# Optimization experiments

Hardware: AMD Instinct MI355X
Metric: run time of the kernel (lower is better)

The kernel has to match this reference:

```python
import jax, jax.numpy as jnp
import numpy as np

# --- static configuration (Octo-base-ish) ---
B, H, MAXH = 2, 5, 10
NT, NP, NW, NR = 16, 256, 64, 1   # task-lang, obs-primary, obs-wrist, readout tokens
DIN, D, NH, DH = 512, 768, 12, 64
L, DF = 12, 3072
PT = NP + NW + NR                  # tokens per timestep
S = NT + H * PT                    # total sequence length = 1621


def _ln(x, s, b):
    m = x.mean(-1, keepdims=True)
    v = ((x - m) ** 2).mean(-1, keepdims=True)
    return (x - m) * jax.lax.rsqrt(v + 1e-6) * s + b


def _pattern():
    # group ids: 0=task, 1=obs_primary, 2=obs_wrist, 3=readout_action
    gid = np.concatenate([np.zeros(NT, np.int32),
                          np.tile(np.concatenate([np.full(NP, 1), np.full(NW, 2), np.full(NR, 3)]).astype(np.int32), H)])
    ts = np.concatenate([np.full(NT, -1, np.int32), np.repeat(np.arange(H, dtype=np.int32), PT)])
    # attention rules: task->task; obs->{task,obs}; readout->{task,obs,own readout}; nobody attends readouts
    R = np.array([[1, 0, 0, 0],
                  [1, 1, 1, 0],
                  [1, 1, 1, 0],
                  [1, 1, 1, 1]], dtype=bool)
    return jnp.asarray(R[gid[:, None], gid[None, :]] & (ts[None, :] <= ts[:, None]))


def setup_inputs() -> dict:
    key = jax.random.key(0)
    ks = iter(jax.random.split(key, 40))
    n = lambda shape, s=0.02: jax.random.normal(next(ks), shape, jnp.float32) * s
    return dict(
        task_tokens=n((B, NT, DIN), 1.0),
        obs_primary=n((B, H, NP, DIN), 1.0),
        obs_wrist=n((B, H, NW, DIN), 1.0),
        W_task=n((DIN, D)), b_task=jnp.zeros((D,)),
        W_primary=n((DIN, D)), b_primary=jnp.zeros((D,)),
        W_wrist=n((DIN, D)), b_wrist=jnp.zeros((D,)),
        pos_task=n((1, NT, D)), pos_primary=n((1, MAXH, NP, D)),
        pos_wrist=n((1, MAXH, NW, D)), pos_readout=n((1, MAXH, NR, D)),
        ln1_s=jnp.ones((L, D)), ln1_b=jnp.zeros((L, D)),
        Wq=n((L, D, D)), bq=jnp.zeros((L, D)),
        Wk=n((L, D, D)), bk=jnp.zeros((L, D)),
        Wv=n((L, D, D)), bv=jnp.zeros((L, D)),
        Wo=n((L, D, D)), bo=jnp.zeros((L, D)),
        ln2_s=jnp.ones((L, D)), ln2_b=jnp.zeros((L, D)),
        W1=n((L, D, DF)), b1=jnp.zeros((L, DF)),
        W2=n((L, DF, D)), b2=jnp.zeros((L, D)),
        lnf_s=jnp.ones((D,)), lnf_b=jnp.zeros((D,)),
        pad_mask=jnp.ones((B, H), jnp.bool_),
    )


def reference(task_tokens, obs_primary, obs_wrist,
              W_task, b_task, W_primary, b_primary, W_wrist, b_wrist,
              pos_task, pos_primary, pos_wrist, pos_readout,
              ln1_s, ln1_b, Wq, bq, Wk, bk, Wv, bv, Wo, bo,
              ln2_s, ln2_b, W1, b1, W2, b2, lnf_s, lnf_b, pad_mask):
    # --- token group assembly: project + positional embed each group ---
    task_e = task_tokens @ W_task + b_task + pos_task                       # [B,NT,D]
    prim_e = obs_primary @ W_primary + b_primary + pos_primary[:, :H]       # [B,H,NP,D]
    wrist_e = obs_wrist @ W_wrist + b_wrist + pos_wrist[:, :H]              # [B,H,NW,D]
    ro_e = jnp.broadcast_to(pos_readout[:, :H], (B, H, NR, D))              # zeros + pos emb
    step = jnp.concatenate([prim_e, wrist_e, ro_e], axis=2).reshape(B, H * PT, D)
    x = jnp.concatenate([task_e, step], axis=1)                             # [B,S,D]
    # --- key validity mask (pad_mask applies to obs groups; readouts always valid) ---
    km_step = jnp.concatenate([
        jnp.broadcast_to(pad_mask[:, :, None], (B, H, NP + NW)),
        jnp.ones((B, H, NR), bool)], axis=2).reshape(B, H * PT)
    key_mask = jnp.concatenate([jnp.ones((B, NT), bool), km_step], axis=1)  # [B,S]
    mask = _pattern()[None] & key_mask[:, None, :]                          # [B,S,S]
    scale = np.float32(1.0 / np.sqrt(DH))

    params = (ln1_s, ln1_b, Wq, bq, Wk, bk, Wv, bv, Wo, bo, ln2_s, ln2_b, W1, b1, W2, b2)

    def block(h, p):
        s1, t1, wq, bq_, wk, bk_, wv, bv_, wo, bo_, s2, t2, w1, b1_, w2, b2_ = p
        y = _ln(h, s1, t1)
        q = (y @ wq + bq_).reshape(B, S, NH, DH)
        k = (y @ wk + bk_).reshape(B, S, NH, DH)
        v = (y @ wv + bv_).reshape(B, S, NH, DH)
        sc = jnp.einsum('bqhd,bkhd->bhqk', q, k) * scale
        sc = jnp.where(mask[:, None], sc, jnp.float32(-1e9))
        a = jax.nn.softmax(sc, axis=-1)
        o = jnp.einsum('bhqk,bkhd->bqhd', a, v).reshape(B, S, D)
        h = h + o @ wo + bo_
        y2 = _ln(h, s2, t2)
        h = h + jax.nn.gelu(y2 @ w1 + b1_) @ w2 + b2_
        return h, None

    x, _ = jax.lax.scan(block, x, params)
    return _ln(x, lnf_s, lnf_b)  # [B,S,D]: [task | per-t (obs_primary, obs_wrist, readout)]
```

## Files before the change

kernel.cpp:

```cpp
#include <hip/hip_runtime.h>
#include <hip/hip_bf16.h>
#include <math.h>

#define Bb   2
#define Hh   5
#define NTT  16
#define NPP  256
#define NWW  64
#define NRR  1
#define PTT  321
#define SS   1621
#define SSP  1664
#define DINN 512
#define DD   768
#define NHH  12
#define DHH  64
#define LL   12
#define DFF  3072
#define MM   3242
#define MPAD 3328
#define QKVN 2304
#define EROWS 3232

typedef __hip_bfloat16 bf16;
typedef _Float16 f16;
typedef __attribute__((ext_vector_type(4))) float  f32x4;
typedef __attribute__((ext_vector_type(8))) __bf16 bf16x8;
typedef __attribute__((ext_vector_type(8))) _Float16 f16x8;

__device__ __forceinline__ void gid_ts(int i, int& g, int& t) {
  if (i < NTT) { g = 0; t = -1; }
  else {
    int j = i - NTT;
    t = j / PTT;
    int r = j - t * PTT;
    g = (r < NPP) ? 1 : ((r < NPP + NWW) ? 2 : 3);
  }
}

template<int ACT, int RES, int OUTBF, int QKVMODE>
__global__ __launch_bounds__(256) void gemm64_k(
    const bf16* __restrict__ A, const bf16* __restrict__ BT,
    const float* __restrict__ bias, const float* __restrict__ Rs,
    void* __restrict__ Cout, f16* __restrict__ VTg,
    int M, int N, int K)
{
  __shared__ bf16 Al[2][64 * 64];
  __shared__ bf16 Bl[2][64 * 64];
  const int tid = threadIdx.x;
  const int lane = tid & 63, w = tid >> 6;
  const int wr = w >> 1, wc = w & 1;
  int bxi = blockIdx.x, byi = blockIdx.y;
  {
    const int nwg = gridDim.x * gridDim.y;
    if ((nwg & 7) == 0) {
      int id = byi * gridDim.x + bxi;
      int swz = (id & 7) * (nwg >> 3) + (id >> 3);
      bxi = swz % gridDim.x; byi = swz / gridDim.x;
    }
  }
  const int bm = byi * 64, bn = bxi * 64;
  const int r0 = lane & 15, kg4 = lane >> 4;
  f32x4 acc[2][2] = {};

  auto STAGE = [&](int s, int k0) {
    #pragma unroll
    for (int i = 0; i < 2; ++i) {
      int chunk = i * 256 + tid;
      int row = chunk >> 3, c8 = chunk & 7;
      const bf16* ga = A  + (size_t)(bm + row) * K + (k0 + c8 * 8);
      const bf16* gb = BT + (size_t)(bn + row) * K + (k0 + c8 * 8);
      __builtin_amdgcn_global_load_lds(
          (const __attribute__((address_space(1))) void*)ga,
          (__attribute__((address_space(3))) void*)((char*)Al[s] + chunk * 16), 16, 0, 0);
      __builtin_amdgcn_global_load_lds(
          (const __attribute__((address_space(1))) void*)gb,
          (__attribute__((address_space(3))) void*)((char*)Bl[s] + chunk * 16), 16, 0, 0);
    }
  };

  const int nt = K >> 6;
  STAGE(0, 0);
  __syncthreads();
  int cur = 0;
  for (int t = 0; t < nt; ++t) {
    if (t + 1 < nt) STAGE(cur ^ 1, (t + 1) << 6);
    #pragma unroll
    for (int ks = 0; ks < 2; ++ks) {
      bf16x8 af[2], bfr[2];
      const int koff = ks * 32 + kg4 * 8;
      #pragma unroll
      for (int mi = 0; mi < 2; ++mi)
        af[mi] = *(const bf16x8*)((const void*)(Al[cur] + (wr * 32 + mi * 16 + r0) * 64 + koff));
      #pragma unroll
      for (int ni = 0; ni < 2; ++ni)
        bfr[ni] = *(const bf16x8*)((const void*)(Bl[cur] + (wc * 32 + ni * 16 + r0) * 64 + koff));
      #pragma unroll
      for (int mi = 0; mi < 2; ++mi)
        #pragma unroll
        for (int ni = 0; ni < 2; ++ni)
          acc[mi][ni] = __builtin_amdgcn_mfma_f32_16x16x32_bf16(af[mi], bfr[ni], acc[mi][ni], 0, 0, 0);
    }
    __syncthreads();
    cur ^= 1;
  }
  #pragma unroll
  for (int mi = 0; mi < 2; ++mi) {
    #pragma unroll
    for (int ni = 0; ni < 2; ++ni) {
      const int gcol = bn + wc * 32 + ni * 16 + r0;
      const float bv = bias[gcol];
      const int gr0 = bm + wr * 32 + mi * 16 + kg4 * 4;
      #pragma unroll
      for (int j = 0; j < 4; ++j) {
        const int gm = gr0 + j;
        if (gm >= M) continue;
        float vv = acc[mi][ni][j] + bv;
        if (ACT == 1) {
          float xx = vv;
          float th = tanhf(0.7978845608028654f * (xx + 0.044715f * xx * xx * xx));
          vv = 0.5f * xx * (1.f + th);
        }
        if (RES) vv += Rs[(size_t)gm * N + gcol];
        if (QKVMODE && gcol >= 1536) {
          const int vc = gcol - 1536;
          const int hh = vc >> 6, d = vc & 63;
          const int bb = gm >= SS;
          const int s = gm - bb * SS;
          VTg[(size_t)((bb * NHH + hh) * 64 + d) * SSP + s] = (f16)vv;
        } else if (OUTBF) {
          ((bf16*)Cout)[(size_t)gm * N + gcol] = __float2bfloat16(vv);
        } else {
          ((float*)Cout)[(size_t)gm * N + gcol] = vv;
        }
      }
    }
  }
}

template<int OUTBF>
__global__ __launch_bounds__(256) void ln2_k(
    const float* __restrict__ X, const float* __restrict__ sc,
    const float* __restrict__ bi, void* __restrict__ Y)
{
  const int row = blockIdx.x;
  const float* x = X + (size_t)row * DD;
  const int t = threadIdx.x;
  float v0 = x[t], v1 = x[t + 256], v2 = x[t + 512];
  float sum = v0 + v1 + v2;
  const int lane = t & 63, wid = t >> 6;
  __shared__ float rs[4];
  #pragma unroll
  for (int o = 32; o; o >>= 1) sum += __shfl_xor(sum, o);
  if (lane == 0) rs[wid] = sum;
  __syncthreads();
  float mean = (rs[0] + rs[1] + rs[2] + rs[3]) * (1.f / DD);
  __syncthreads();
  float d0 = v0 - mean, d1 = v1 - mean, d2 = v2 - mean;
  float sq = d0 * d0 + d1 * d1 + d2 * d2;
  #pragma unroll
  for (int o = 32; o; o >>= 1) sq += __shfl_xor(sq, o);
  if (lane == 0) rs[wid] = sq;
  __syncthreads();
  float var = (rs[0] + rs[1] + rs[2] + rs[3]) * (1.f / DD);
  float inv = rsqrtf(var + 1e-6f);
  float o0 = d0 * inv * sc[t] + bi[t];
  float o1 = d1 * inv * sc[t + 256] + bi[t + 256];
  float o2 = d2 * inv * sc[t + 512] + bi[t + 512];
  if (OUTBF) {
    bf16* y = (bf16*)Y + (size_t)row * DD;
    y[t] = __float2bfloat16(o0); y[t + 256] = __float2bfloat16(o1); y[t + 512] = __float2bfloat16(o2);
  } else {
    float* y = (float*)Y + (size_t)row * DD;
    y[t] = o0; y[t + 256] = o1; y[t + 512] = o2;
  }
}

__global__ __launch_bounds__(256) void mattn_k(
    const bf16* __restrict__ qkv, const f16* __restrict__ VTg,
    bf16* __restrict__ ao, const unsigned char* __restrict__ kflags)
{
  __shared__ bf16 Kl[2][64 * 64];
  __shared__ f16  Vl[2][64 * 64];
  __shared__ unsigned short Pl[4][16][72];
  __shared__ unsigned char Fl[2][64];
  const int tid = threadIdx.x;
  const int lane = tid & 63, w = tid >> 6;
  const int r0 = lane & 15, g = lane >> 4;
  int swz;
  {
    int id = blockIdx.x;
    swz = (id & 7) * 78 + (id >> 3);
  }
  const int qt = swz % 26;
  const int hb = swz / 26;
  const int h = hb % NHH, b = hb / NHH;

  const int q_my = qt * 64 + w * 16 + r0;
  const int qc = min(q_my, SS - 1);
  int gq, tq; gid_ts(qc, gq, tq);
  const int kend = (tq < 0) ? NTT : NTT + (tq + 1) * PTT;
  const bool gq3 = (gq == 3);

  const int qlast = min(qt * 64 + 63, SS - 1);
  int gl, tl; gid_ts(qlast, gl, tl);
  const int kend_b = (tl < 0) ? NTT : NTT + (tl + 1) * PTT;
  const int ntiles = (kend_b + 63) >> 6;

  bf16x8 qf[2];
  {
    const bf16* qrow = qkv + (size_t)(b * SS + qc) * QKVN + h * DHH;
    qf[0] = *(const bf16x8*)((const void*)(qrow + g * 8));
    qf[1] = *(const bf16x8*)((const void*)(qrow + 32 + g * 8));
  }

  auto STAGE = [&](int s, int kt) {
    const int kv0 = kt * 64;
    #pragma unroll
    for (int i = 0; i < 2; ++i) {
      int c = i * 256 + tid;
      int row = c >> 3, blk = c & 7;
      int srow = min(kv0 + row, SS - 1);
      const bf16* srcK = qkv + (size_t)(b * SS + srow) * QKVN + DD + h * DHH + ((blk ^ (row & 7)) * 8);
      __builtin_amdgcn_global_load_lds(
          (const __attribute__((address_space(1))) void*)srcK,
          (__attribute__((address_space(3))) void*)((char*)Kl[s] + c * 16), 16, 0, 0);
      int kvs = kv0 + ((blk ^ (row & 7)) * 8);
      const f16* srcV = VTg + (size_t)((b * NHH + h) * 64 + row) * SSP + kvs;
      __builtin_amdgcn_global_load_lds(
          (const __attribute__((address_space(1))) void*)srcV,
          (__attribute__((address_space(3))) void*)((char*)Vl[s] + c * 16), 16, 0, 0);
    }
    if (tid < 64) Fl[s][tid] = kflags[b * SS + min(kv0 + tid, SS - 1)];
  };

  f32x4 o_acc[4] = {};
  float l_run = 0.f;

  STAGE(0, 0);
  __syncthreads();
  int cur = 0;
  for (int kt = 0; kt < ntiles; ++kt) {
    const int kv0 = kt * 64;
    if (kt + 1 < ntiles) STAGE(cur ^ 1, kt + 1);

    f32x4 st[4] = {};
    #pragma unroll
    for (int ks = 0; ks < 2; ++ks) {
      #pragma unroll
      for (int t = 0; t < 4; ++t) {
        const int krow = t * 16 + r0;
        const bf16x8 af = *(const bf16x8*)((const void*)(
            (char*)Kl[cur] + krow * 128 + ((ks * 64 + g * 16) ^ ((krow & 7) << 4))));
        st[t] = __builtin_amdgcn_mfma_f32_16x16x32_bf16(af, qf[ks], st[t], 0, 0, 0);
      }
    }
    #pragma unroll
    for (int t = 0; t < 4; ++t) {
      const unsigned fl4 = *(const unsigned*)((const void*)&Fl[cur][t * 16 + g * 4]);
      unsigned short pk[4];
      #pragma unroll
      for (int r = 0; r < 4; ++r) {
        const int kg_ = kv0 + t * 16 + g * 4 + r;
        const unsigned fb = (fl4 >> (8 * r)) & 0xffu;
        const bool ok = (kg_ < kend) && (fb & 1) && (gq3 || !(fb & 2));
        float ee = fminf(fmaf(st[t][r], 0.125f, -2.0f), 10.0f);
        float pv = ok ? __expf(ee) : 0.f;
        f16 hb2 = (f16)pv;
        l_run += (float)hb2;
        pk[r] = *(unsigned short*)&hb2;
      }
      uint2 pw;
      pw.x = (unsigned)pk[0] | ((unsigned)pk[1] << 16);
      pw.y = (unsigned)pk[2] | ((unsigned)pk[3] << 16);
      *(uint2*)((void*)&Pl[w][r0][t * 16 + g * 4]) = pw;
    }
    asm volatile("s_waitcnt lgkmcnt(0)" ::: "memory");
    __builtin_amdgcn_sched_barrier(0);
    #pragma unroll
    for (int ks = 0; ks < 2; ++ks) {
      const f16x8 pa = *(const f16x8*)((const void*)(
          (char*)&Pl[w][r0][0] + ks * 64 + g * 16));
      #pragma unroll
      for (int n = 0; n < 4; ++n) {
        const int drow = n * 16 + r0;
        const f16x8 bv = *(const f16x8*)((const void*)(
            (char*)Vl[cur] + drow * 128 + ((ks * 64 + g * 16) ^ ((drow & 7) << 4))));
        o_acc[n] = __builtin_amdgcn_mfma_f32_16x16x32_f16(pa, bv, o_acc[n], 0, 0, 0);
      }
    }
    __syncthreads();
    cur ^= 1;
  }
  float lt = l_run;
  lt += __shfl_xor(lt, 16);
  lt += __shfl_xor(lt, 32);
  const float inv = 1.f / lt;
  float invr[4];
  #pragma unroll
  for (int j = 0; j < 4; ++j) invr[j] = __shfl(inv, g * 4 + j);
  #pragma unroll
  for (int n = 0; n < 4; ++n) {
    const int d = n * 16 + r0;
    #pragma unroll
    for (int j = 0; j < 4; ++j) {
      const int q = qt * 64 + w * 16 + g * 4 + j;
      if (q < SS)
        ao[(size_t)(b * SS + q) * DD + h * DHH + d] = __float2bfloat16(o_acc[n][j] * invr[j]);
    }
  }
}

__global__ __launch_bounds__(256) void assemble_k(
    const float* __restrict__ tE, const float* __restrict__ pE, const float* __restrict__ wE,
    const float* __restrict__ posT, const float* __restrict__ posP,
    const float* __restrict__ posW, const float* __restrict__ posR,
    float* __restrict__ X)
{
  const int row = blockIdx.x;
  const int b = row / SS, s = row - b * SS;
  float* x = X + (size_t)row * DD;
  const float* src; const float* pos;
  if (s < NTT) { src = tE + (size_t)(b * NTT + s) * DD; pos = posT + (size_t)s * DD; }
  else {
    int j = s - NTT, t = j / PTT, r = j - t * PTT;
    if (r < NPP)            { src = pE + (size_t)((b * Hh + t) * NPP + r) * DD;
                              pos = posP + (size_t)(t * NPP + r) * DD; }
    else if (r < NPP + NWW) { src = wE + (size_t)((b * Hh + t) * NWW + (r - NPP)) * DD;
                              pos = posW + (size_t)(t * NWW + (r - NPP)) * DD; }
    else                    { src = nullptr; pos = posR + (size_t)t * DD; }
  }
  for (int d = threadIdx.x; d < DD; d += 256)
    x[d] = (src ? src[d] : 0.f) + pos[d];
}

__global__ void build_kv_k(const void* pm, unsigned char* kvout) {
  int i = blockIdx.x * 256 + threadIdx.x;
  if (i >= Bb * SS) return;
  int b = i / SS, s = i - b * SS;
  int g, t; gid_ts(s, g, t);
  unsigned char valid = 1;
  if (g == 1 || g == 2) {
    int idx = b * Hh + t;
    unsigned char c = ((const unsigned char*)pm)[idx];
    int ii = ((const int*)pm)[idx];
    valid = (c != 0 || ii != 0) ? 1 : 0;
  }
  kvout[i] = valid | ((g == 3) ? 2 : 0);
}

__global__ void zset_k(ushort4* p, int n16) {
  int i = blockIdx.x * 256 + threadIdx.x;
  if (i < n16) { ushort4 z = {0, 0, 0, 0}; p[i] = z; }
}

__global__ __launch_bounds__(256) void eprep_k(
    const float* __restrict__ Wt, const float* __restrict__ Wp, const float* __restrict__ Ww,
    bf16* __restrict__ ET)
{
  const int bid = blockIdx.x;
  const int sel = bid / 384, rem = bid % 384;
  const int a = rem / 24, bcol = rem % 24;
  const float* src = sel == 0 ? Wt : (sel == 1 ? Wp : Ww);
  bf16* dst = ET + (size_t)sel * 768 * 512;
  __shared__ float t[32][33];
  const int ib = threadIdx.x >> 5, j = threadIdx.x & 31;
  #pragma unroll
  for (int rr = 0; rr < 4; ++rr) {
    int i = ib + rr * 8;
    t[i][j] = src[(size_t)(a * 32 + i) * 768 + bcol * 32 + j];
  }
  __syncthreads();
  #pragma unroll
  for (int rr = 0; rr < 4; ++rr) {
    int i = ib + rr * 8;
    dst[(size_t)(bcol * 32 + i) * 512 + a * 32 + j] = __float2bfloat16(t[j][i]);
  }
}

__global__ void cvtA_k(const float* __restrict__ t, const float* __restrict__ p,
                       const float* __restrict__ w, bf16* __restrict__ out)
{
  int i = blockIdx.x * 256 + threadIdx.x;
  const int total4 = EROWS * 512 / 4;
  if (i >= total4) return;
  int e = i * 4;
  const float* src; int off;
  if (e < 32 * 512)        { src = t; off = e; }
  else if (e < 2592 * 512) { src = p; off = e - 32 * 512; }
  else                     { src = w; off = e - 2592 * 512; }
  float4 v = *(const float4*)(src + off);
  bf16* o = out + e;
  o[0] = __float2bfloat16(v.x); o[1] = __float2bfloat16(v.y);
  o[2] = __float2bfloat16(v.z); o[3] = __float2bfloat16(v.w);
}

__global__ __launch_bounds__(256) void prep_k(
    const float* __restrict__ Wq, const float* __restrict__ Wk, const float* __restrict__ Wv,
    const float* __restrict__ Wo, const float* __restrict__ W1, const float* __restrict__ W2,
    bf16* __restrict__ QKVT, bf16* __restrict__ OT,
    bf16* __restrict__ W1T, bf16* __restrict__ W2T,
    const float* __restrict__ bq_, const float* __restrict__ bk_,
    const float* __restrict__ bv_, float* __restrict__ bqkv)
{
  const int bid = blockIdx.x;
  if (bid >= 6912) {
    int i = (bid - 6912) * 256 + threadIdx.x;
    if (i < QKVN) bqkv[i] = (i < DD) ? bq_[i] : ((i < 2 * DD) ? bk_[i - DD] : bv_[i - 2 * DD]);
    return;
  }
  __shared__ float t[32][33];
  const float* src; bf16* dst;
  int a, bcol, R, C, dbase;
  if (bid < 1728)      { int sel = bid / 576, rem = bid % 576; a = rem / 24; bcol = rem % 24;
                         src = sel == 0 ? Wq : (sel == 1 ? Wk : Wv);
                         dst = QKVT; R = 768; C = 768; dbase = sel * 768; }
  else if (bid < 2304) { int rem = bid - 1728; a = rem / 24; bcol = rem % 24;
                         src = Wo; dst = OT; R = 768; C = 768; dbase = 0; }
  else if (bid < 4608) { int rem = bid - 2304; a = rem / 96; bcol = rem % 96;
                         src = W1; dst = W1T; R = 768; C = 3072; dbase = 0; }
  else                 { int rem = bid - 4608; a = rem / 24; bcol = rem % 24;
                         src = W2; dst = W2T; R = 3072; C = 768; dbase = 0; }
  const int ib = threadIdx.x >> 5, j = threadIdx.x & 31;
  #pragma unroll
  for (int rr = 0; rr < 4; ++rr) {
    int i = ib + rr * 8;
    t[i][j] = src[(size_t)(a * 32 + i) * C + bcol * 32 + j];
  }
  __syncthreads();
  #pragma unroll
  for (int rr = 0; rr < 4; ++rr) {
    int i = ib + rr * 8;
    dst[(size_t)(dbase + bcol * 32 + i) * R + a * 32 + j] = __float2bfloat16(t[j][i]);
  }
}

extern "C" void kernel_launch(void* const* d_in, const int* in_sizes, int n_in,
                              void* d_out, int out_size, void* d_ws, size_t ws_size,
                              hipStream_t stream)
{
  const float* task_tokens = (const float*)d_in[0];
  const float* obs_primary = (const float*)d_in[1];
  const float* obs_wrist   = (const float*)d_in[2];
  const float* W_task      = (const float*)d_in[3];
  const float* b_task      = (const float*)d_in[4];
  const float* W_primary   = (const float*)d_in[5];
  const float* b_primary   = (const float*)d_in[6];
  const float* W_wrist     = (const float*)d_in[7];
  const float* b_wrist     = (const float*)d_in[8];
  const float* pos_task    = (const float*)d_in[9];
  const float* pos_primary = (const float*)d_in[10];
  const float* pos_wrist   = (const float*)d_in[11];
  const float* pos_readout = (const float*)d_in[12];
  const float* ln1_s = (const float*)d_in[13];
  const float* ln1_b = (const float*)d_in[14];
  const float* Wq = (const float*)d_in[15];
  const float* bq = (const float*)d_in[16];
  const float* Wk = (const float*)d_in[17];
  const float* bk = (const float*)d_in[18];
  const float* Wv = (const float*)d_in[19];
  const float* bv = (const float*)d_in[20];
  const float* Wo = (const float*)d_in[21];
  const float* bo = (const float*)d_in[22];
  const float* ln2_s = (const float*)d_in[23];
  const float* ln2_b = (const float*)d_in[24];
  const float* W1 = (const float*)d_in[25];
  const float* b1 = (const float*)d_in[26];
  const float* W2 = (const float*)d_in[27];
  const float* b2 = (const float*)d_in[28];
  const float* lnf_s = (const float*)d_in[29];
  const float* lnf_b = (const float*)d_in[30];
  const void*  pad_mask = d_in[31];

  char* p = (char*)d_ws;
  auto alloc = [&](size_t bytes) { char* r = p; p += (bytes + 255) & ~(size_t)255; return r; };
  float* x    = (float*)alloc((size_t)MPAD * DD * 4);
  bf16*  y    = (bf16*) alloc((size_t)MPAD * DD * 2);
  bf16*  qkv  = (bf16*) alloc((size_t)MPAD * QKVN * 2);
  bf16*  ao   = (bf16*) alloc((size_t)MPAD * DD * 2);
  f16*   VTg  = (f16*)  alloc((size_t)Bb * NHH * 64 * SSP * 2);
  bf16*  QKVT = (bf16*) alloc((size_t)QKVN * DD * 2);
  bf16*  OT   = (bf16*) alloc((size_t)DD * DD * 2);
  bf16*  W1T  = (bf16*) alloc((size_t)DFF * DD * 2);
  bf16*  W2T  = (bf16*) alloc((size_t)DD * DFF * 2);
  bf16*  ET   = (bf16*) alloc((size_t)3 * DD * DINN * 2);
  bf16*  abf  = (bf16*) alloc((size_t)EROWS * DINN * 2);
  float* bqkv = (float*)alloc(QKVN * 4);
  unsigned char* keyv = (unsigned char*)alloc(Bb * SS);
  char* uni = alloc((size_t)MPAD * DFF * 2);
  bf16*  h1   = (bf16*)uni;
  float* te   = (float*)uni;
  float* pe   = te + (size_t)Bb * NTT * DD;
  float* we   = pe + (size_t)Bb * Hh * NPP * DD;

  {
    int n16 = (int)((size_t)Bb * NHH * 64 * SSP * 2 / 16);
    zset_k<<<dim3((n16 + 255) / 256), 256, 0, stream>>>((ushort4*)VTg, n16);
  }
  eprep_k<<<1152, 256, 0, stream>>>(W_task, W_primary, W_wrist, ET);
  cvtA_k<<<dim3((EROWS * 512 / 4 + 255) / 256), 256, 0, stream>>>(
      task_tokens, obs_primary, obs_wrist, abf);
  gemm64_k<0, 0, 0, 0><<<dim3(12, 1),  256, 0, stream>>>(
      abf,              ET,                 b_task,    nullptr, te, nullptr, 32,          DD, DINN);
  gemm64_k<0, 0, 0, 0><<<dim3(12, 40), 256, 0, stream>>>(
      abf + 32 * DINN,  ET + DD * DINN,     b_primary, nullptr, pe, nullptr, 2560,        DD, DINN);
  gemm64_k<0, 0, 0, 0><<<dim3(12, 10), 256, 0, stream>>>(
      abf + 2592 * DINN, ET + 2 * DD * DINN, b_wrist,  nullptr, we, nullptr, 640,         DD, DINN);
  assemble_k<<<dim3(MM), 256, 0, stream>>>(te, pe, we, pos_task, pos_primary, pos_wrist, pos_readout, x);
  build_kv_k<<<dim3((Bb * SS + 255) / 256), 256, 0, stream>>>(pad_mask, keyv);

  for (int l = 0; l < LL; ++l) {
    prep_k<<<6921, 256, 0, stream>>>(
        Wq + (size_t)l * DD * DD, Wk + (size_t)l * DD * DD, Wv + (size_t)l * DD * DD,
        Wo + (size_t)l * DD * DD, W1 + (size_t)l * DD * DFF, W2 + (size_t)l * DFF * DD,
        QKVT, OT, W1T, W2T,
        bq + l * DD, bk + l * DD, bv + l * DD, bqkv);
    ln2_k<1><<<MM, 256, 0, stream>>>(x, ln1_s + l * DD, ln1_b + l * DD, y);
    gemm64_k<0, 0, 1, 1><<<dim3(QKVN / 64, MPAD / 64), 256, 0, stream>>>(
        y, QKVT, bqkv, nullptr, qkv, VTg, MM, QKVN, DD);
    mattn_k<<<dim3(26 * NHH * Bb), 256, 0, stream>>>(qkv, VTg, ao, keyv);
    gemm64_k<0, 1, 0, 0><<<dim3(DD / 64, MPAD / 64), 256, 0, stream>>>(
        ao, OT, bo + l * DD, x, x, nullptr, MM, DD, DD);
    ln2_k<1><<<MM, 256, 0, stream>>>(x, ln2_s + l * DD, ln2_b + l * DD, y);
    gemm64_k<1, 0, 1, 0><<<dim3(DFF / 64, MPAD / 64), 256, 0, stream>>>(
        y, W1T, b1 + l * DFF, nullptr, h1, nullptr, MM, DFF, DD);
    gemm64_k<0, 1, 0, 0><<<dim3(DD / 64, MPAD / 64), 256, 0, stream>>>(
        h1, W2T, b2 + l * DD, x, x, nullptr, MM, DD, DFF);
  }
  ln2_k<0><<<MM, 256, 0, stream>>>(x, lnf_s, lnf_b, d_out);
}
```

Baseline: 2.661 ms.

## Split-K the N=768 GEMMs, fuse residual reduction with LayerNorm, batch weight prep

The Wo and W2 projections (N=768, few tiles) now run split-K (2 and 4 ways), writing fp32 partials. A new kernel sums the partials, bias and residual, then applies the next LayerNorm. This fuses the residual update with ln2, ln1 of the next layer, or the final LN. All twelve layers' weight transposes are also done in one launch up front instead of per layer. The aim is to fill more CUs on the skinny GEMMs and cut launch and extra passes, at the cost of extra partial-buffer traffic and more workspace.

Measured after the change: 2.779 ms. 1.04x slower.

```diff
diff --git a/kernel.cpp b/kernel.cpp
--- a/kernel.cpp
+++ b/kernel.cpp
@@ -38,7 +38,7 @@
   }
 }
 
-template<int ACT, int RES, int OUTBF, int QKVMODE>
+template<int ACT, int RES, int OUTBF, int QKVMODE, int SPLIT>
 __global__ __launch_bounds__(256) void gemm64_k(
     const bf16* __restrict__ A, const bf16* __restrict__ BT,
     const float* __restrict__ bias, const float* __restrict__ Rs,
@@ -61,6 +61,9 @@
   }
   const int bm = byi * 64, bn = bxi * 64;
   const int r0 = lane & 15, kg4 = lane >> 4;
+  const int ksub = SPLIT ? (K / SPLIT) : K;
+  const int kbase = SPLIT ? blockIdx.z * ksub : 0;
+  float* Cp = SPLIT ? ((float*)Cout + (size_t)blockIdx.z * MPAD * N) : (float*)Cout;
   f32x4 acc[2][2] = {};
 
   auto STAGE = [&](int s, int k0) {
@@ -68,8 +71,8 @@
     for (int i = 0; i < 2; ++i) {
       int chunk = i * 256 + tid;
       int row = chunk >> 3, c8 = chunk & 7;
-      const bf16* ga = A  + (size_t)(bm + row) * K + (k0 + c8 * 8);
-      const bf16* gb = BT + (size_t)(bn + row) * K + (k0 + c8 * 8);
+      const bf16* ga = A  + (size_t)(bm + row) * K + (kbase + k0 + c8 * 8);
+      const bf16* gb = BT + (size_t)(bn + row) * K + (kbase + k0 + c8 * 8);
       __builtin_amdgcn_global_load_lds(
           (const __attribute__((address_space(1))) void*)ga,
           (__attribute__((address_space(3))) void*)((char*)Al[s] + chunk * 16), 16, 0, 0);
@@ -79,7 +82,7 @@
     }
   };
 
-  const int nt = K >> 6;
+  const int nt = ksub >> 6;
   STAGE(0, 0);
   __syncthreads();
   int cur = 0;
@@ -131,17 +134,64 @@
         } else if (OUTBF) {
           ((bf16*)Cout)[(size_t)gm * N + gcol] = __float2bfloat16(vv);
         } else {
-          ((float*)Cout)[(size_t)gm * N + gcol] = vv;
+          Cp[(size_t)gm * N + gcol] = vv;
         }
       }
     }
   }
 }
 
-template<int OUTBF>
+template<int NS, int FINAL>
+__global__ __launch_bounds__(256) void comb_ln_k(
+    const float* __restrict__ pacc, const float* __restrict__ bias,
+    float* __restrict__ x, const float* __restrict__ sc,
+    const float* __restrict__ bi, void* __restrict__ Y)
+{
+  const int row = blockIdx.x;
+  const int t = threadIdx.x;
+  float v[3];
+  #pragma unroll
+  for (int j = 0; j < 3; ++j) {
+    const int d = t + j * 256;
+    float s = x[(size_t)row * DD + d] + bias[d];
+    #pragma unroll
+    for (int ns = 0; ns < NS; ++ns)
+      s += pacc[(size_t)ns * MPAD * DD + (size_t)row * DD + d];
+    v[j] = s;
+    if (!FINAL) x[(size_t)row * DD + d] = s;
+  }
+  const int lane = t & 63, wid = t >> 6;
+  __shared__ float rs[4];
+  float sum = v[0] + v[1] + v[2];
+  #pragma unroll
+  for (int o = 32; o; o >>= 1) sum += __shfl_xor(sum, o);
+  if (lane == 0) rs[wid] = sum;
+  __syncthreads();
+  float mean = (rs[0] + rs[1] + rs[2] + rs[3]) * (1.f / DD);
+  __syncthreads();
+  float d0 = v[0] - mean, d1 = v[1] - mean, d2 = v[2] - mean;
+  float sq = d0 * d0 + d1 * d1 + d2 * d2;
+  #pragma unroll
+  for (int o = 32; o; o >>= 1) sq += __shfl_xor(sq, o);
+  if (lane == 0) rs[wid] = sq;
+  __syncthreads();
+  float var = (rs[0] + rs[1] + rs[2] + rs[3]) * (1.f / DD);
+  float inv = rsqrtf(var + 1e-6f);
+  float o0 = d0 * inv * sc[t] + bi[t];
+  float o1 = d1 * inv * sc[t + 256] + bi[t + 256];
+  float o2 = d2 * inv * sc[t + 512] + bi[t + 512];
+  if (FINAL) {
+    float* y = (float*)Y + (size_t)row * DD;
+    y[t] = o0; y[t + 256] = o1; y[t + 512] = o2;
+  } else {
+    bf16* y = (bf16*)Y + (size_t)row * DD;
+    y[t] = __float2bfloat16(o0); y[t + 256] = __float2bfloat16(o1); y[t + 512] = __float2bfloat16(o2);
+  }
+}
+
 __global__ __launch_bounds__(256) void ln2_k(
     const float* __restrict__ X, const float* __restrict__ sc,
-    const float* __restrict__ bi, void* __restrict__ Y)
+    const float* __restrict__ bi, bf16* __restrict__ Y)
 {
   const int row = blockIdx.x;
   const float* x = X + (size_t)row * DD;
@@ -164,16 +214,10 @@
   __syncthreads();
   float var = (rs[0] + rs[1] + rs[2] + rs[3]) * (1.f / DD);
   float inv = rsqrtf(var + 1e-6f);
-  float o0 = d0 * inv * sc[t] + bi[t];
-  float o1 = d1 * inv * sc[t + 256] + bi[t + 256];
-  float o2 = d2 * inv * sc[t + 512] + bi[t + 512];
-  if (OUTBF) {
-    bf16* y = (bf16*)Y + (size_t)row * DD;
-    y[t] = __float2bfloat16(o0); y[t + 256] = __float2bfloat16(o1); y[t + 512] = __float2bfloat16(o2);
-  } else {
-    float* y = (float*)Y + (size_t)row * DD;
-    y[t] = o0; y[t + 256] = o1; y[t + 512] = o2;
-  }
+  bf16* y = Y + (size_t)row * DD;
+  y[t]       = __float2bfloat16(d0 * inv * sc[t] + bi[t]);
+  y[t + 256] = __float2bfloat16(d1 * inv * sc[t + 256] + bi[t + 256]);
+  y[t + 512] = __float2bfloat16(d2 * inv * sc[t + 512] + bi[t + 512]);
 }
 
 __global__ __launch_bounds__(256) void mattn_k(
@@ -395,7 +439,7 @@
   o[2] = __float2bfloat16(v.z); o[3] = __float2bfloat16(v.w);
 }
 
-__global__ __launch_bounds__(256) void prep_k(
+__global__ __launch_bounds__(256) void prep12_k(
     const float* __restrict__ Wq, const float* __restrict__ Wk, const float* __restrict__ Wv,
     const float* __restrict__ Wo, const float* __restrict__ W1, const float* __restrict__ W2,
     bf16* __restrict__ QKVT, bf16* __restrict__ OT,
@@ -403,24 +447,32 @@
     const float* __restrict__ bq_, const float* __restrict__ bk_,
     const float* __restrict__ bv_, float* __restrict__ bqkv)
 {
-  const int bid = blockIdx.x;
+  const int l = blockIdx.x / 6921;
+  const int bid = blockIdx.x % 6921;
   if (bid >= 6912) {
     int i = (bid - 6912) * 256 + threadIdx.x;
-    if (i < QKVN) bqkv[i] = (i < DD) ? bq_[i] : ((i < 2 * DD) ? bk_[i - DD] : bv_[i - 2 * DD]);
+    if (i < QKVN) {
+      float v = (i < DD) ? bq_[l * DD + i]
+              : ((i < 2 * DD) ? bk_[l * DD + i - DD] : bv_[l * DD + i - 2 * DD]);
+      bqkv[l * QKVN + i] = v;
+    }
     return;
   }
   __shared__ float t[32][33];
   const float* src; bf16* dst;
   int a, bcol, R, C, dbase;
   if (bid < 1728)      { int sel = bid / 576, rem = bid % 576; a = rem / 24; bcol = rem % 24;
-                         src = sel == 0 ? Wq : (sel == 1 ? Wk : Wv);
-                         dst = QKVT; R = 768; C = 768; dbase = sel * 768; }
+                         src = (sel == 0 ? Wq : (sel == 1 ? Wk : Wv)) + (size_t)l * DD * DD;
+                         dst = QKVT + (size_t)l * QKVN * DD; R = 768; C = 768; dbase = sel * 768; }
   else if (bid < 2304) { int rem = bid - 1728; a = rem / 24; bcol = rem % 24;
-                         src = Wo; dst = OT; R = 768; C = 768; dbase = 0; }
+                         src = Wo + (size_t)l * DD * DD; dst = OT + (size_t)l * DD * DD;
+                         R = 768; C = 768; dbase = 0; }
   else if (bid < 4608) { int rem = bid - 2304; a = rem / 96; bcol = rem % 96;
-                         src = W1; dst = W1T; R = 768; C = 3072; dbase = 0; }
+                         src = W1 + (size_t)l * DD * DFF; dst = W1T + (size_t)l * DFF * DD;
+                         R = 768; C = 3072; dbase = 0; }
   else                 { int rem = bid - 4608; a = rem / 24; bcol = rem % 24;
-                         src = W2; dst = W2T; R = 3072; C = 768; dbase = 0; }
+                         src = W2 + (size_t)l * DFF * DD; dst = W2T + (size_t)l * DD * DFF;
+                         R = 3072; C = 768; dbase = 0; }
   const int ib = threadIdx.x >> 5, j = threadIdx.x & 31;
   #pragma unroll
   for (int rr = 0; rr < 4; ++rr) {
@@ -479,13 +531,16 @@
   bf16*  qkv  = (bf16*) alloc((size_t)MPAD * QKVN * 2);
   bf16*  ao   = (bf16*) alloc((size_t)MPAD * DD * 2);
   f16*   VTg  = (f16*)  alloc((size_t)Bb * NHH * 64 * SSP * 2);
-  bf16*  QKVT = (bf16*) alloc((size_t)QKVN * DD * 2);
-  bf16*  OT   = (bf16*) alloc((size_t)DD * DD * 2);
-  bf16*  W1T  = (bf16*) alloc((size_t)DFF * DD * 2);
-  bf16*  W2T  = (bf16*) alloc((size_t)DD * DFF * 2);
+  bf16*  QKVT = (bf16*) alloc((size_t)LL * QKVN * DD * 2);
+  bf16*  OT   = (bf16*) alloc((size_t)LL * DD * DD * 2);
+  bf16*  W1T  = (bf16*) alloc((size_t)LL * DFF * DD * 2);
+  bf16*  W2T  = (bf16*) alloc((size_t)LL * DD * DFF * 2);
   bf16*  ET   = (bf16*) alloc((size_t)3 * DD * DINN * 2);
   bf16*  abf  = (bf16*) alloc((size_t)EROWS * DINN * 2);
-  float* bqkv = (float*)alloc(QKVN * 4);
+  float* bqkv = (float*)alloc((size_t)LL * QKVN * 4);
+  float* po   = (float*)alloc((size_t)2 * MPAD * DD * 4);
+  float* pw   = (float*)alloc((size_t)4 * MPAD * DD * 4);
+  float* zbuf = (float*)alloc(DD * 4);
   unsigned char* keyv = (unsigned char*)alloc(Bb * SS);
   char* uni = alloc((size_t)MPAD * DFF * 2);
   bf16*  h1   = (bf16*)uni;
@@ -496,36 +551,39 @@
   {
     int n16 = (int)((size_t)Bb * NHH * 64 * SSP * 2 / 16);
     zset_k<<<dim3((n16 + 255) / 256), 256, 0, stream>>>((ushort4*)VTg, n16);
-  }
+    zset_k<<<dim3(1), 256, 0, stream>>>((ushort4*)zbuf, DD * 4 / 16);
+  }
+  prep12_k<<<LL * 6921, 256, 0, stream>>>(Wq, Wk, Wv, Wo, W1, W2,
+                                          QKVT, OT, W1T, W2T, bq, bk, bv, bqkv);
   eprep_k<<<1152, 256, 0, stream>>>(W_task, W_primary, W_wrist, ET);
   cvtA_k<<<dim3((EROWS * 512 / 4 + 255) / 256), 256, 0, stream>>>(
       task_tokens, obs_primary, obs_wrist, abf);
-  gemm64_k<0, 0, 0, 0><<<dim3(12, 1),  256, 0, stream>>>(
-      abf,              ET,                 b_task,    nullptr, te, nullptr, 32,          DD, DINN);
-  gemm64_k<0, 0, 0, 0><<<dim3(12, 40), 256, 0, stream>>>(
-      abf + 32 * DINN,  ET + DD * DINN,     b_primary, nullptr, pe, nullptr, 2560,        DD, DINN);
-  gemm64_k<0, 0, 0, 0><<<dim3(12, 10), 256, 0, stream>>>(
-      abf + 2592 * DINN, ET + 2 * DD * DINN, b_wrist,  nullptr, we, nullptr, 640,         DD, DINN);
+  gemm64_k<0, 0, 0, 0, 0><<<dim3(12, 1),  256, 0, stream>>>(
+      abf,               ET,                 b_task,    nullptr, te, nullptr, 32,   DD, DINN);
+  gemm64_k<0, 0, 0, 0, 0><<<dim3(12, 40), 256, 0, stream>>>(
+      abf + 32 * DINN,   ET + DD * DINN,     b_primary, nullptr, pe, nullptr, 2560, DD, DINN);
+  gemm64_k<0, 0, 0, 0, 0><<<dim3(12, 10), 256, 0, stream>>>(
+      abf + 2592 * DINN, ET + 2 * DD * DINN, b_wrist,   nullptr, we, nullptr, 640,  DD, DINN);
   assemble_k<<<dim3(MM), 256, 0, stream>>>(te, pe, we, pos_task, pos_primary, pos_wrist, pos_readout, x);
   build_kv_k<<<dim3((Bb * SS + 255) / 256), 256, 0, stream>>>(pad_mask, keyv);
+  ln2_k<<<MM, 256, 0, stream>>>(x, ln1_s, ln1_b, y);
 
   for (int l = 0; l < LL; ++l) {
-    prep_k<<<6921, 256, 0, stream>>>(
-        Wq + (size_t)l * DD * DD, Wk + (size_t)l * DD * DD, Wv + (size_t)l * DD * DD,
-        Wo + (size_t)l * DD * DD, W1 + (size_t)l * DD * DFF, W2 + (size_t)l * DFF * DD,
-        QKVT, OT, W1T, W2T,
-        bq + l * DD, bk + l * DD, bv + l * DD, bqkv);
-    ln2_k<1><<<MM, 256, 0, stream>>>(x, ln1_s + l * DD, ln1_b + l * DD, y);
-    gemm64_k<0, 0, 1, 1><<<dim3(QKVN / 64, MPAD / 64), 256, 0, stream>>>(
-        y, QKVT, bqkv, nullptr, qkv, VTg, MM, QKVN, DD);
+    gemm64_k<0, 0, 1, 1, 0><<<dim3(QKVN / 64, MPAD / 64), 256, 0, stream>>>(
+        y, QKVT + (size_t)l * QKVN * DD, bqkv + l * QKVN, nullptr, qkv, VTg, MM, QKVN, DD);
     mattn_k<<<dim3(26 * NHH * Bb), 256, 0, stream>>>(qkv, VTg, ao, keyv);
-    gemm64_k<0, 1, 0, 0><<<dim3(DD / 64, MPAD / 64), 256, 0, stream>>>(
-        ao, OT, bo + l * DD, x, x, nullptr, MM, DD, DD);
-    ln2_k<1><<<MM, 256, 0, stream>>>(x, ln2_s + l * DD, ln2_b + l * DD, y);
-    gemm64_k<1, 0, 1, 0><<<dim3(DFF / 64, MPAD / 64), 256, 0, stream>>>(
-        y, W1T, b1 + l * DFF, nullptr, h1, nullptr, MM, DFF, DD);
-    gemm64_k<0, 1, 0, 0><<<dim3(DD / 64, MPAD / 64), 256, 0, stream>>>(
-        h1, W2T, b2 + l * DD, x, x, nullptr, MM, DD, DFF);
-  }
-  ln2_k<0><<<MM, 256, 0, stream>>>(x, lnf_s, lnf_b, d_out);
-}
+    gemm64_k<0, 0, 0, 0, 2><<<dim3(DD / 64, MPAD / 64, 2), 256, 0, stream>>>(
+        ao, OT + (size_t)l * DD * DD, zbuf, nullptr, po, nullptr, MM, DD, DD);
+    comb_ln_k<2, 0><<<MM, 256, 0, stream>>>(po, bo + l * DD, x,
+                                            ln2_s + l * DD, ln2_b + l * DD, y);
+    gemm64_k<1, 0, 1, 0, 0><<<dim3(DFF / 64, MPAD / 64), 256, 0, stream>>>(
+        y, W1T + (size_t)l * DFF * DD, b1 + l * DFF, nullptr, h1, nullptr, MM, DFF, DD);
+    gemm64_k<0, 0, 0, 0, 4><<<dim3(DD / 64, MPAD / 64, 4), 256, 0, stream>>>(
+        h1, W2T + (size_t)l * DD * DFF, zbuf, nullptr, pw, nullptr, MM, DD, DFF);
+    if (l < LL - 1)
+      comb_ln_k<4, 0><<<MM, 256, 0, stream>>>(pw, b2 + l * DD, x,
+                                              ln1_s + (l + 1) * DD, ln1_b + (l + 1) * DD, y);
+    else
+      comb_ln_k<4, 1><<<MM, 256, 0, stream>>>(pw, b2 + l * DD, x, lnf_s, lnf_b, d_out);
+  }
+}
```
